# Performance work log

Measured on AMD Instinct MI355X. Metric: run time of the kernel, lower is better.

## Reference

```python
import jax, jax.numpy as jnp
import numpy as np

KERNEL = 8
WEIGHT_INIT = np.array([0.49403, -0.44625, 0.82544, 0.99267, 1.6915, -2.0835, 2.9114,
                        -5.6555, 3.5984, -10.205, 20.828, -0.0022237, 0.0097854, 157.35],
                       dtype=np.float32)


def setup_inputs() -> dict:
    key = jax.random.key(0)
    x = jax.random.normal(key, (2048, 128, KERNEL, KERNEL), dtype=jnp.float32)
    weight = jnp.asarray(WEIGHT_INIT)
    return {"input": x, "weight": weight}


def reference(input, weight):
    eye = jnp.eye(KERNEL, dtype=input.dtype)  # serves as both mask and eye(8)
    # A = I - x @ x^T  over trailing two dims
    A = eye - jnp.matmul(input, jnp.swapaxes(input, 2, 3))
    B = jnp.matmul(A, A)
    C = jnp.matmul(B, A)
    D = jnp.matmul(C, A)
    E = jnp.matmul(D, A)
    F = jnp.matmul(E, A)
    G = jnp.matmul(F, A)
    Mat = (weight[0] * A + weight[1] * B + weight[2] * C + weight[3] * D
           + weight[4] * E + weight[5] * F + weight[6] * G + weight[7] * eye)
    return input + jnp.matmul(Mat, input)
```

## Files before the change

### kernel.cpp

```cpp
#include <hip/hip_runtime.h>


__global__ __launch_bounds__(256, 2)
void ns_poly_kernel(const float* __restrict__ in,
                    const float* __restrict__ wp,
                    float* __restrict__ out)
{
    const int tid = threadIdx.x;
    const int m   = blockIdx.x * 128 + (tid >> 1);
    const int h   = tid & 1;

    const float* xm = in  + (size_t)m * 64 + (size_t)h * 32;
    float*       om = out + (size_t)m * 64 + (size_t)h * 32;

    const float w0 = wp[0], w1 = wp[1], w2 = wp[2], w3 = wp[3];
    const float w4 = wp[4], w5 = wp[5], w6 = wp[6], w7 = wp[7];

    float x[4][8];
#pragma unroll
    for (int r = 0; r < 4; ++r) {
        const float4 a = reinterpret_cast<const float4*>(xm)[2 * r];
        const float4 b = reinterpret_cast<const float4*>(xm)[2 * r + 1];
        x[r][0] = a.x; x[r][1] = a.y; x[r][2] = a.z; x[r][3] = a.w;
        x[r][4] = b.x; x[r][5] = b.y; x[r][6] = b.z; x[r][7] = b.w;
    }

    float xo[4][8];
#pragma unroll
    for (int r = 0; r < 4; ++r)
#pragma unroll
        for (int j = 0; j < 8; ++j)
            xo[r][j] = __shfl_xor(x[r][j], 1);

    float A[4][8];
#pragma unroll
    for (int i = 0; i < 4; ++i) {
#pragma unroll
        for (int c = 0; c < 4; ++c) {
            if (c < i) continue;
            float s = x[i][0] * x[c][0];
#pragma unroll
            for (int k = 1; k < 8; ++k) s += x[i][k] * x[c][k];
            const float v = (i == c ? 1.0f : 0.0f) - s;
            A[i][c] = v;
            A[c][i] = v;
        }
#pragma unroll
        for (int r = 0; r < 4; ++r) {
            float s = x[i][0] * xo[r][0];
#pragma unroll
            for (int k = 1; k < 8; ++k) s += x[i][k] * xo[r][k];
            A[i][4 + r] = -s;
        }
    }

    float t[4][8];
#pragma unroll
    for (int i = 0; i < 4; ++i)
#pragma unroll
        for (int j = 0; j < 8; ++j)
            t[i][j] = w6 * x[i][j];

    auto horner_step = [&](float wk) {
        float to[4][8];
#pragma unroll
        for (int r = 0; r < 4; ++r)
#pragma unroll
            for (int j = 0; j < 8; ++j)
                to[r][j] = __shfl_xor(t[r][j], 1);
        float tn[4][8];
#pragma unroll
        for (int i = 0; i < 4; ++i)
#pragma unroll
            for (int j = 0; j < 8; ++j) {
                float s = wk * x[i][j];
#pragma unroll
                for (int r = 0; r < 4; ++r) s += A[i][r]     * t[r][j];
#pragma unroll
                for (int r = 0; r < 4; ++r) s += A[i][4 + r] * to[r][j];
                tn[i][j] = s;
            }
#pragma unroll
        for (int i = 0; i < 4; ++i)
#pragma unroll
            for (int j = 0; j < 8; ++j)
                t[i][j] = tn[i][j];
    };

    horner_step(w5);
    horner_step(w4);
    horner_step(w3);
    horner_step(w2);
    horner_step(w1);
    horner_step(w0);

    {
        float to[4][8];
#pragma unroll
        for (int r = 0; r < 4; ++r)
#pragma unroll
            for (int j = 0; j < 8; ++j)
                to[r][j] = __shfl_xor(t[r][j], 1);
        const float wf = 1.0f + w7;
#pragma unroll
        for (int i = 0; i < 4; ++i) {
            float o[8];
#pragma unroll
            for (int j = 0; j < 8; ++j) {
                float s = wf * x[i][j];
#pragma unroll
                for (int r = 0; r < 4; ++r) s += A[i][r]     * t[r][j];
#pragma unroll
                for (int r = 0; r < 4; ++r) s += A[i][4 + r] * to[r][j];
                o[j] = s;
            }
            reinterpret_cast<float4*>(om)[2 * i]     = make_float4(o[0], o[1], o[2], o[3]);
            reinterpret_cast<float4*>(om)[2 * i + 1] = make_float4(o[4], o[5], o[6], o[7]);
        }
    }
}

extern "C" void kernel_launch(void* const* d_in, const int* in_sizes, int n_in,
                              void* d_out, int out_size, void* d_ws, size_t ws_size,
                              hipStream_t stream)
{
    const float* in = (const float*)d_in[0];
    const float* w  = (const float*)d_in[1];
    float* out      = (float*)d_out;

    const int nmat   = in_sizes[0] / 64;
    const int blocks = nmat / 128;
    ns_poly_kernel<<<blocks, 256, 0, stream>>>(in, w, out);
}
```

Before: 130.7 us.

## Split matrices by columns per lane to remove shuffles from Horner steps

Each lane pair now splits the 8x8 matrix by columns instead of rows. The full symmetric A is formed from partial Gram sums exchanged once, and each lane stores A in packed upper-triangular form (36 values). Horner steps then need no cross-lane shuffles, and the final step is folded in as one more Horner iteration. Launch bounds rise to 4 blocks per CU to allow higher occupancy, at the cost of register pressure and a transpose plus shuffle on load and store.

```diff
diff --git a/kernel.cpp b/kernel.cpp
--- a/kernel.cpp
+++ b/kernel.cpp
@@ -1,7 +1,13 @@
 #include <hip/hip_runtime.h>
 
 
-__global__ __launch_bounds__(256, 2)
+__device__ __forceinline__ constexpr int sidx(int a, int b) {
+    const int i = a < b ? a : b;
+    const int k = a < b ? b : a;
+    return i * 8 - i * (i + 1) / 2 + k;
+}
+
+__global__ __launch_bounds__(256, 4)
 void ns_poly_kernel(const float* __restrict__ in,
                     const float* __restrict__ wp,
                     float* __restrict__ out)
@@ -9,82 +15,80 @@
     const int tid = threadIdx.x;
     const int m   = blockIdx.x * 128 + (tid >> 1);
     const int h   = tid & 1;
-
-    const float* xm = in  + (size_t)m * 64 + (size_t)h * 32;
-    float*       om = out + (size_t)m * 64 + (size_t)h * 32;
+    const bool hb = (h != 0);
 
     const float w0 = wp[0], w1 = wp[1], w2 = wp[2], w3 = wp[3];
     const float w4 = wp[4], w5 = wp[5], w6 = wp[6], w7 = wp[7];
 
-    float x[4][8];
+    const float* xm = in + (size_t)m * 64 + (size_t)h * 32;
+    float xr[4][8];
 #pragma unroll
     for (int r = 0; r < 4; ++r) {
         const float4 a = reinterpret_cast<const float4*>(xm)[2 * r];
         const float4 b = reinterpret_cast<const float4*>(xm)[2 * r + 1];
-        x[r][0] = a.x; x[r][1] = a.y; x[r][2] = a.z; x[r][3] = a.w;
-        x[r][4] = b.x; x[r][5] = b.y; x[r][6] = b.z; x[r][7] = b.w;
+        xr[r][0] = a.x; xr[r][1] = a.y; xr[r][2] = a.z; xr[r][3] = a.w;
+        xr[r][4] = b.x; xr[r][5] = b.y; xr[r][6] = b.z; xr[r][7] = b.w;
     }
 
-    float xo[4][8];
+    float xc[4][8];
+#pragma unroll
+    for (int p = 0; p < 4; ++p)
+#pragma unroll
+        for (int jj = 0; jj < 4; ++jj)
+            xc[jj][p] = hb ? xr[p][4 + jj] : xr[p][jj];
 #pragma unroll
     for (int r = 0; r < 4; ++r)
 #pragma unroll
-        for (int j = 0; j < 8; ++j)
-            xo[r][j] = __shfl_xor(x[r][j], 1);
+        for (int jj = 0; jj < 4; ++jj) {
+            const float sv = hb ? xr[r][jj] : xr[r][4 + jj];
+            xc[jj][4 + r] = __shfl_xor(sv, 1);
+        }
 
-    float A[4][8];
+    float S[36];
 #pragma unroll
-    for (int i = 0; i < 4; ++i) {
+    for (int p = 0; p < 8; ++p)
 #pragma unroll
-        for (int c = 0; c < 4; ++c) {
-            if (c < i) continue;
-            float s = x[i][0] * x[c][0];
+        for (int q = 0; q < 8; ++q) {
+            if (q < p) continue;
+            float s = xc[0][p] * xc[0][q];
+            s += xc[1][p] * xc[1][q];
+            s += xc[2][p] * xc[2][q];
+            s += xc[3][p] * xc[3][q];
+            S[sidx(p, q)] = s;
+        }
+    float A[36];
 #pragma unroll
-            for (int k = 1; k < 8; ++k) s += x[i][k] * x[c][k];
-            const float v = (i == c ? 1.0f : 0.0f) - s;
-            A[i][c] = v;
-            A[c][i] = v;
+    for (int p = 0; p < 8; ++p)
+#pragma unroll
+        for (int q = 0; q < 8; ++q) {
+            if (q < p) continue;
+            const float other = __shfl_xor(S[sidx((p + 4) & 7, (q + 4) & 7)], 1);
+            A[sidx(p, q)] = (p == q ? 1.0f : 0.0f) - S[sidx(p, q)] - other;
         }
-#pragma unroll
-        for (int r = 0; r < 4; ++r) {
-            float s = x[i][0] * xo[r][0];
-#pragma unroll
-            for (int k = 1; k < 8; ++k) s += x[i][k] * xo[r][k];
-            A[i][4 + r] = -s;
-        }
-    }
 
     float t[4][8];
 #pragma unroll
-    for (int i = 0; i < 4; ++i)
+    for (int jj = 0; jj < 4; ++jj)
 #pragma unroll
-        for (int j = 0; j < 8; ++j)
-            t[i][j] = w6 * x[i][j];
+        for (int p = 0; p < 8; ++p)
+            t[jj][p] = w6 * xc[jj][p];
 
     auto horner_step = [&](float wk) {
-        float to[4][8];
 #pragma unroll
-        for (int r = 0; r < 4; ++r)
+        for (int jj = 0; jj < 4; ++jj) {
+            float s[8];
 #pragma unroll
-            for (int j = 0; j < 8; ++j)
-                to[r][j] = __shfl_xor(t[r][j], 1);
-        float tn[4][8];
+            for (int p = 0; p < 8; ++p)
+                s[p] = wk * xc[jj][p];
 #pragma unroll
-        for (int i = 0; i < 4; ++i)
+            for (int q = 0; q < 8; ++q)
 #pragma unroll
-            for (int j = 0; j < 8; ++j) {
-                float s = wk * x[i][j];
+                for (int p = 0; p < 8; ++p)
+                    s[p] += A[sidx(p, q)] * t[jj][q];
 #pragma unroll
-                for (int r = 0; r < 4; ++r) s += A[i][r]     * t[r][j];
-#pragma unroll
-                for (int r = 0; r < 4; ++r) s += A[i][4 + r] * to[r][j];
-                tn[i][j] = s;
-            }
-#pragma unroll
-        for (int i = 0; i < 4; ++i)
-#pragma unroll
-            for (int j = 0; j < 8; ++j)
-                t[i][j] = tn[i][j];
+            for (int p = 0; p < 8; ++p)
+                t[jj][p] = s[p];
+        }
     };
 
     horner_step(w5);
@@ -93,30 +97,26 @@
     horner_step(w2);
     horner_step(w1);
     horner_step(w0);
+    horner_step(1.0f + w7);
 
-    {
-        float to[4][8];
+    float rv[4][4];
+#pragma unroll
+    for (int jj = 0; jj < 4; ++jj)
 #pragma unroll
         for (int r = 0; r < 4; ++r)
+            rv[jj][r] = __shfl_xor(t[jj][4 + r], 1);
+
+    float* om = out + (size_t)m * 64 + (size_t)h * 32;
 #pragma unroll
-            for (int j = 0; j < 8; ++j)
-                to[r][j] = __shfl_xor(t[r][j], 1);
-        const float wf = 1.0f + w7;
+    for (int r = 0; r < 4; ++r) {
+        float o[8];
 #pragma unroll
-        for (int i = 0; i < 4; ++i) {
-            float o[8];
-#pragma unroll
-            for (int j = 0; j < 8; ++j) {
-                float s = wf * x[i][j];
-#pragma unroll
-                for (int r = 0; r < 4; ++r) s += A[i][r]     * t[r][j];
-#pragma unroll
-                for (int r = 0; r < 4; ++r) s += A[i][4 + r] * to[r][j];
-                o[j] = s;
-            }
-            reinterpret_cast<float4*>(om)[2 * i]     = make_float4(o[0], o[1], o[2], o[3]);
-            reinterpret_cast<float4*>(om)[2 * i + 1] = make_float4(o[4], o[5], o[6], o[7]);
+        for (int c = 0; c < 4; ++c) {
+            o[c]     = hb ? rv[c][r] : t[c][r];
+            o[4 + c] = hb ? t[c][r] : rv[c][r];
         }
+        reinterpret_cast<float4*>(om)[2 * r]     = make_float4(o[0], o[1], o[2], o[3]);
+        reinterpret_cast<float4*>(om)[2 * r + 1] = make_float4(o[4], o[5], o[6], o[7]);
     }
 }
 
@@ -126,9 +126,9 @@
 {
     const float* in = (const float*)d_in[0];
     const float* w  = (const float*)d_in[1];
-    float* out      = (float*)d_out;
+    float* outp     = (float*)d_out;
 
     const int nmat   = in_sizes[0] / 64;
     const int blocks = nmat / 128;
-    ns_poly_kernel<<<blocks, 256, 0, stream>>>(in, w, out);
+    ns_poly_kernel<<<blocks, 256, 0, stream>>>(in, w, outp);
 }
```

Result: slower. 280.8 us (+114.8%).
